# Performance work log

Measured on AMD Instinct MI355X. Metric: run time of the kernel, lower is better.

The kernel has to match this reference:

```python
import jax, jax.numpy as jnp
import numpy as np

N = 100000   # nodes
E = 1600000  # edges (avg degree 16)
F = 128      # num_node_features
H = 128      # hid_size
G = 512      # num graphs in batch
C = 10       # num_classes
D = 32       # graph_degree_distribution.shape[1]
BN_EPS = 1e-5


def setup_inputs() -> dict:
    key = jax.random.key(0)
    ks = jax.random.split(key, 16)
    p = lambda k, shp: jax.random.normal(k, shp, jnp.float32) * 0.02
    x = jax.random.normal(ks[0], (N, F), jnp.float32)
    edge_index = jax.random.randint(ks[1], (2, E), 0, N)
    batch = jnp.sort(jax.random.randint(ks[2], (N,), 0, G))
    degree = jax.random.uniform(ks[3], (N,), jnp.float32) * 10.0
    return dict(
        x=x, edge_index=edge_index, batch=batch, degree=degree,
        eps1=jnp.zeros(()), W1a=p(ks[4], (F, H)), b1a=jnp.zeros(H), W1b=p(ks[5], (H, H)), b1b=jnp.zeros(H),
        g1=jnp.ones(H), be1=jnp.zeros(H),
        eps2=jnp.zeros(()), W2a=p(ks[6], (H, H)), b2a=jnp.zeros(H), W2b=p(ks[7], (H, H)), b2b=jnp.zeros(H),
        g2=jnp.ones(H), be2=jnp.zeros(H),
        Wlin1=p(ks[8], (H, H)), blin1=jnp.zeros(H),
        Wlin2=p(ks[9], (H, C)), blin2=jnp.zeros(C),
        Wlin4=p(ks[10], (H, D)), blin4=jnp.zeros(D),
        Wloss=p(ks[11], (H, 1)), bloss=jnp.zeros(1),
    )


def gin_conv(x, src, dst, eps, Wa, ba, Wb, bb, gamma, beta):
    # GINConv: MLP((1+eps)*x_i + sum_{j->i} x_j); MLP = Lin-ReLU-Lin-ReLU-BN
    agg = jax.ops.segment_sum(x[src], dst, num_segments=x.shape[0])  # [N,F] gather-scatter
    h = (1.0 + eps) * x + agg
    h = jax.nn.relu(h @ Wa + ba)
    h = jax.nn.relu(h @ Wb + bb)
    mu = h.mean(0)
    var = h.var(0)  # biased var, training-mode BN
    return gamma * (h - mu) * jax.lax.rsqrt(var + BN_EPS) + beta


def reference(x, edge_index, batch, degree,
              eps1, W1a, b1a, W1b, b1b, g1, be1,
              eps2, W2a, b2a, W2b, b2b, g2, be2,
              Wlin1, blin1, Wlin2, blin2, Wlin4, blin4, Wloss, bloss):
    src, dst = edge_index[0], edge_index[1]
    h = gin_conv(x, src, dst, eps1, W1a, b1a, W1b, b1b, g1, be1)
    h = gin_conv(h, src, dst, eps2, W2a, b2a, W2b, b2b, g2, be2)
    mse_x = h @ Wloss + bloss                       # [N,1]
    mse_loss = jnp.mean((mse_x - degree[:, None]) ** 2)
    # global_mean_pool over graphs
    sums = jax.ops.segment_sum(h, batch, num_segments=G)
    cnts = jax.ops.segment_sum(jnp.ones((h.shape[0], 1), h.dtype), batch, num_segments=G)
    g = sums / jnp.maximum(cnts, 1.0)               # [G,H]
    z = jax.nn.relu(g @ Wlin1 + blin1)              # dropout inert (eval)
    result1 = jax.nn.log_softmax(z @ Wlin2 + blin2, axis=-1)  # [G,C]
    result3 = z @ Wlin4 + blin4                      # [G,D]
    return result1, result3, mse_loss
```

## Files before the change

### kernel.cpp

```cpp
#include <hip/hip_runtime.h>
#include <hip/hip_bf16.h>

#define HF 128
#define BSH 8
#define BSZ 256
#define NBMAX 1024
#define FCAP 8192
#define HB 512

typedef __attribute__((ext_vector_type(8))) short bf16x8;
typedef __attribute__((ext_vector_type(4))) float f32x4;
typedef __attribute__((ext_vector_type(2))) float f32x2;

__device__ inline float bflo(unsigned u) { return __uint_as_float(u << 16); }
__device__ inline float bfhi(unsigned u) { return __uint_as_float(u & 0xffff0000u); }
__device__ inline unsigned short f2bf(float f) {
    unsigned u = __float_as_uint(f);
    unsigned r = (u + 0x7fffu + ((u >> 16) & 1u)) >> 16;
    return (unsigned short)r;
}
__device__ inline unsigned pack2(float a, float b) {
    return (unsigned)f2bf(a) | ((unsigned)f2bf(b) << 16);
}
__device__ inline uint2 pk8_fp8(const float* v) {
    int a = __builtin_amdgcn_cvt_pk_fp8_f32(v[0], v[1], 0, 0);
    a = __builtin_amdgcn_cvt_pk_fp8_f32(v[2], v[3], a, 1);
    int b = __builtin_amdgcn_cvt_pk_fp8_f32(v[4], v[5], 0, 0);
    b = __builtin_amdgcn_cvt_pk_fp8_f32(v[6], v[7], b, 1);
    uint2 r; r.x = (unsigned)a; r.y = (unsigned)b;
    return r;
}

__global__ __launch_bounds__(256) void init_all(
    const float* __restrict__ x, unsigned short* __restrict__ xb,
    unsigned char* __restrict__ x8, int castBlk, int nchunks,
    const float* __restrict__ w0, const float* __restrict__ w1,
    const float* __restrict__ w2, const float* __restrict__ w3,
    unsigned short* __restrict__ WtAll,
    const int* __restrict__ dst, int* __restrict__ tot, int E, int chunkH,
    const int* __restrict__ batch, int* __restrict__ gstart, int N, int Gn, int nBlocks,
    float* __restrict__ Szero, float* __restrict__ outm)
{
    __shared__ int lh[NBMAX];
    int b = blockIdx.x;
    int t = threadIdx.x;
    if (b < castBlk) {
        int i = b * 256 + t;
        if (i < nchunks) {
            float4 a = ((const float4*)x)[2 * i];
            float4 c = ((const float4*)x)[2 * i + 1];
            uint4 o;
            o.x = pack2(a.x, a.y); o.y = pack2(a.z, a.w);
            o.z = pack2(c.x, c.y); o.w = pack2(c.z, c.w);
            ((uint4*)xb)[i] = o;
            float v[8] = {a.x, a.y, a.z, a.w, c.x, c.y, c.z, c.w};
            ((uint2*)x8)[i] = pk8_fp8(v);
        }
        return;
    }
    b -= castBlk;
    if (b < 4) {
        const float* W = (b == 0) ? w0 : (b == 1) ? w1 : (b == 2) ? w2 : w3;
        unsigned short* O = WtAll + b * 16384;
        for (int idx = t; idx < 16384; idx += 256) {
            int j    = idx & 7;
            int lane = (idx >> 3) & 63;
            int fk   = idx >> 9;
            int kk = fk & 3, nt = fk >> 2;
            int m = lane & 15, quad = lane >> 4;
            int ncol = nt * 16 + m;
            int krow = kk * 32 + quad * 8 + j;
            O[idx] = f2bf(W[krow * 128 + ncol]);
        }
        return;
    }
    b -= 4;
    if (b < HB) {
        int NBl = (N + BSZ - 1) >> BSH;
        for (int i = t; i < NBl; i += 256) lh[i] = 0;
        __syncthreads();
        int beg = b * chunkH;
        int end = min(E, beg + chunkH);
        for (int e = beg + t; e < end; e += 256)
            atomicAdd(&lh[dst[e] >> BSH], 1);
        __syncthreads();
        for (int i = t; i < NBl; i += 256) {
            int c = lh[i];
            if (c) atomicAdd(&tot[i], c);
        }
        return;
    }
    b -= HB;
    if (b < nBlocks) {
        int i = b * 256 + t;
        if (i >= N) return;
        int bi = batch[i];
        int bp = (i == 0) ? -1 : batch[i - 1];
        for (int g = bp + 1; g <= bi; g++) gstart[g] = i;
        if (i == N - 1)
            for (int g = bi + 1; g <= Gn; g++) gstart[g] = N;
        return;
    }
    if (t < 2 * HF) { Szero[t] = 0.f; Szero[t + 2 * HF] = 0.f; }
    if (t == 0) outm[0] = 0.f;
}

__global__ void scanp(const int* __restrict__ tot, int* __restrict__ boff,
                      int* __restrict__ bcur, int NB, int E)
{
    __shared__ int part[256];
    int t = threadIdx.x;
    int v[4];
    int s = 0;
#pragma unroll
    for (int i = 0; i < 4; i++) {
        int idx = t * 4 + i;
        v[i] = (idx < NB) ? tot[idx] : 0;
        s += v[i];
    }
    part[t] = s;
    __syncthreads();
    for (int o = 1; o < 256; o <<= 1) {
        int y = (t >= o) ? part[t - o] : 0;
        __syncthreads();
        part[t] += y;
        __syncthreads();
    }
    int base = part[t] - s;
#pragma unroll
    for (int i = 0; i < 4; i++) {
        int idx = t * 4 + i;
        if (idx < NB) { boff[idx] = base; bcur[idx] = base; base += v[i]; }
    }
    if (t == 0) boff[NB] = E;
}

__global__ __launch_bounds__(256) void bucket_bin(
    const int* __restrict__ src, const int* __restrict__ dst,
    int* __restrict__ bcur, unsigned* __restrict__ ebuf, int E, int NB, int chunkH)
{
    __shared__ int lh[NBMAX];
    int t = threadIdx.x;
    for (int i = t; i < NB; i += 256) lh[i] = 0;
    __syncthreads();
    int beg = blockIdx.x * chunkH;
    int end = min(E, beg + chunkH);
    for (int e = beg + t; e < end; e += 256)
        atomicAdd(&lh[dst[e] >> BSH], 1);
    __syncthreads();
    for (int i = t; i < NB; i += 256) {
        int c = lh[i];
        lh[i] = c ? atomicAdd(&bcur[i], c) : 0;
    }
    __syncthreads();
    for (int e = beg + t; e < end; e += 256) {
        int d = dst[e];
        int b = d >> BSH;
        int pos = atomicAdd(&lh[b], 1);
        ebuf[pos] = ((unsigned)src[e] << BSH) | (unsigned)(d & (BSZ - 1));
    }
}

__global__ __launch_bounds__(256) void bucket_fill(
    const unsigned* __restrict__ ebuf, const int* __restrict__ boff,
    int* __restrict__ off, int* __restrict__ esrc, int N, int NB, int E)
{
    __shared__ int deg[BSZ];
    __shared__ int pref[BSZ];
    __shared__ int lcur[BSZ];
    __shared__ int lsr[FCAP];
    int b = blockIdx.x;
    int t = threadIdx.x;
    int segBeg = boff[b], segEnd = boff[b + 1];
    int segLen = segEnd - segBeg;
    int node0 = b << BSH;
    deg[t] = 0;
    __syncthreads();
    for (int i = segBeg + t; i < segEnd; i += 256)
        atomicAdd(&deg[ebuf[i] & (BSZ - 1)], 1);
    __syncthreads();
    int dv = deg[t];
    pref[t] = dv;
    __syncthreads();
    for (int o = 1; o < 256; o <<= 1) {
        int y = (t >= o) ? pref[t - o] : 0;
        __syncthreads();
        pref[t] += y;
        __syncthreads();
    }
    int excl = pref[t] - dv;
    int node = node0 + t;
    if (node < N) off[node] = segBeg + excl;
    lcur[t] = excl;
    if (b == NB - 1 && t == 0) off[N] = E;
    __syncthreads();
    if (segLen <= FCAP) {
        for (int i = segBeg + t; i < segEnd; i += 256) {
            unsigned v = ebuf[i];
            int slot = atomicAdd(&lcur[v & (BSZ - 1)], 1);
            lsr[slot] = (int)(v >> BSH);
        }
        __syncthreads();
        for (int i = t; i < segLen; i += 256) esrc[segBeg + i] = lsr[i];
    } else {
        for (int i = segBeg + t; i < segEnd; i += 256) {
            unsigned v = ebuf[i];
            int slot = atomicAdd(&lcur[v & (BSZ - 1)], 1);
            esrc[segBeg + slot] = (int)(v >> BSH);
        }
    }
}

template <bool FOLD>
__global__ __launch_bounds__(256, 4) void gather_u(
    const unsigned short* __restrict__ xb, const unsigned char* __restrict__ x8,
    const int* __restrict__ off, const int* __restrict__ esrc,
    const float* __restrict__ epsp,
    const float* __restrict__ S1, const float* __restrict__ S2,
    const float* __restrict__ gamma, const float* __restrict__ beta, float invN,
    unsigned short* __restrict__ Uo, int N)
{
    __shared__ float lsc[HF], lsh[HF];
    int tid = threadIdx.x;
    if (FOLD) {
        if (tid < HF) {
            float mu = S1[tid] * invN;
            float var = S2[tid] * invN - mu * mu;
            float rs = rsqrtf(var + 1e-5f);
            float sc = gamma[tid] * rs;
            lsc[tid] = sc;
            lsh[tid] = beta[tid] - mu * sc;
        }
        __syncthreads();
    }
    int lane16 = tid & 15;
    int node = (blockIdx.x * 256 + tid) >> 4;
    if (node >= N) return;
    int beg = off[node], end = off[node + 1];
    float acc[8] = {0.f, 0.f, 0.f, 0.f, 0.f, 0.f, 0.f, 0.f};
    const unsigned char* x8l = x8 + lane16 * 8;
    for (int j0 = beg; j0 < end; j0 += 16) {
        int myidx = (j0 + lane16 < end) ? esrc[j0 + lane16] : -1;
        uint2 pb[16];
#pragma unroll
        for (int t = 0; t < 16; t++) {
            int s = __shfl(myidx, t, 16);
            int sc = (s < 0) ? 0 : s;
            uint2 pv = *(const uint2*)(x8l + (size_t)sc * HF);
            if (s < 0) { pv.x = 0u; pv.y = 0u; }
            pb[t] = pv;
        }
#pragma unroll
        for (int t = 0; t < 16; t++) {
            f32x2 f0 = __builtin_amdgcn_cvt_pk_f32_fp8((int)pb[t].x, 0);
            f32x2 f1 = __builtin_amdgcn_cvt_pk_f32_fp8((int)pb[t].x, 1);
            f32x2 f2 = __builtin_amdgcn_cvt_pk_f32_fp8((int)pb[t].y, 0);
            f32x2 f3 = __builtin_amdgcn_cvt_pk_f32_fp8((int)pb[t].y, 1);
            acc[0] += f0.x; acc[1] += f0.y;
            acc[2] += f1.x; acc[3] += f1.y;
            acc[4] += f2.x; acc[5] += f2.y;
            acc[6] += f3.x; acc[7] += f3.y;
        }
    }
    float ep = 1.0f + epsp[0];
    uint4 xx = *(const uint4*)(xb + (size_t)node * HF + lane16 * 8);
    acc[0] += ep * bflo(xx.x); acc[1] += ep * bfhi(xx.x);
    acc[2] += ep * bflo(xx.y); acc[3] += ep * bfhi(xx.y);
    acc[4] += ep * bflo(xx.z); acc[5] += ep * bfhi(xx.z);
    acc[6] += ep * bflo(xx.w); acc[7] += ep * bfhi(xx.w);
    if (FOLD) {
        float cf = ep + (float)(end - beg);
        const float4 s0 = *(const float4*)(&lsc[lane16 * 8]);
        const float4 s1 = *(const float4*)(&lsc[lane16 * 8 + 4]);
        const float4 h0 = *(const float4*)(&lsh[lane16 * 8]);
        const float4 h1 = *(const float4*)(&lsh[lane16 * 8 + 4]);
        acc[0] = acc[0] * s0.x + h0.x * cf; acc[1] = acc[1] * s0.y + h0.y * cf;
        acc[2] = acc[2] * s0.z + h0.z * cf; acc[3] = acc[3] * s0.w + h0.w * cf;
        acc[4] = acc[4] * s1.x + h1.x * cf; acc[5] = acc[5] * s1.y + h1.y * cf;
        acc[6] = acc[6] * s1.z + h1.z * cf; acc[7] = acc[7] * s1.w + h1.w * cf;
    }
    uint4 o;
    o.x = pack2(acc[0], acc[1]); o.y = pack2(acc[2], acc[3]);
    o.z = pack2(acc[4], acc[5]); o.w = pack2(acc[6], acc[7]);
    *(uint4*)(Uo + (size_t)node * HF + lane16 * 8) = o;
}

__global__ __launch_bounds__(256, 4) void gemm2L(
    const unsigned short* __restrict__ U,
    const unsigned short* __restrict__ Wfa, const float* __restrict__ ba,
    const unsigned short* __restrict__ Wfb, const float* __restrict__ bb,
    unsigned short* __restrict__ out, unsigned char* __restrict__ out8,
    float* __restrict__ S1, float* __restrict__ S2, int n)
{
    __shared__ __align__(16) unsigned short lT[8192];
    __shared__ float lS1[HF], lS2[HF];
    int tid = threadIdx.x;
    int w = tid >> 6, lane = tid & 63;
    int m = lane & 15, quad = lane >> 4;
    int tile = (blockIdx.x << 2) | w;
    int ntiles = (n + 15) >> 4;
    bool active = tile < ntiles;

    if (tid < HF) { lS1[tid] = 0.f; lS2[tid] = 0.f; }
    __syncthreads();

    if (active) {
        unsigned short* lTw = lT + w * 2048;
        int swzA = (m & 7) << 3;
        int row0 = tile << 4;

        int ar = row0 + m; if (ar >= n) ar = n - 1;
        const unsigned short* up = U + (size_t)ar * HF + quad * 8;
        bf16x8 aF[4];
#pragma unroll
        for (int kk = 0; kk < 4; kk++) aF[kk] = *(const bf16x8*)(up + kk * 32);

        float bav[8], bbv[8];
#pragma unroll
        for (int nt = 0; nt < 8; nt++) { bav[nt] = ba[nt * 16 + m]; bbv[nt] = bb[nt * 16 + m]; }

        const bf16x8* __restrict__ Ba = (const bf16x8*)Wfa;
        const bf16x8* __restrict__ Bb = (const bf16x8*)Wfb;

        f32x4 acc[8];
#pragma unroll
        for (int nt = 0; nt < 8; nt++) acc[nt] = (f32x4){0.f, 0.f, 0.f, 0.f};
#pragma unroll
        for (int nt = 0; nt < 8; nt++) {
#pragma unroll
            for (int kk = 0; kk < 4; kk++) {
                bf16x8 b = Ba[(((nt << 2) | kk) << 6) | lane];
                acc[nt] = __builtin_amdgcn_mfma_f32_16x16x32_bf16(aF[kk], b, acc[nt], 0, 0, 0);
            }
        }
#pragma unroll
        for (int nt = 0; nt < 8; nt++) {
#pragma unroll
            for (int r = 0; r < 4; r++) {
                int row = (quad << 2) | r;
                lTw[(row << 7) | ((nt * 16 + m) ^ ((row & 7) << 3))] =
                    f2bf(fmaxf(acc[nt][r] + bav[nt], 0.f));
            }
        }
        bf16x8 a2[4];
#pragma unroll
        for (int kk = 0; kk < 4; kk++)
            a2[kk] = *(const bf16x8*)(&lTw[(m << 7) | (((kk << 5) | (quad << 3)) ^ swzA)]);
#pragma unroll
        for (int nt = 0; nt < 8; nt++) acc[nt] = (f32x4){0.f, 0.f, 0.f, 0.f};
#pragma unroll
        for (int nt = 0; nt < 8; nt++) {
#pragma unroll
            for (int kk = 0; kk < 4; kk++) {
                bf16x8 b = Bb[(((nt << 2) | kk) << 6) | lane];
                acc[nt] = __builtin_amdgcn_mfma_f32_16x16x32_bf16(a2[kk], b, acc[nt], 0, 0, 0);
            }
        }
#pragma unroll
        for (int nt = 0; nt < 8; nt++) {
            float cs = 0.f, cq = 0.f;
#pragma unroll
            for (int r = 0; r < 4; r++) {
                int row = (quad << 2) | r;
                float v = fmaxf(acc[nt][r] + bbv[nt], 0.f);
                lTw[(row << 7) | ((nt * 16 + m) ^ ((row & 7) << 3))] = f2bf(v);
                if (row0 + row < n) { cs += v; cq += v * v; }
            }
            cs += __shfl_down(cs, 32); cs += __shfl_down(cs, 16);
            cq += __shfl_down(cq, 32); cq += __shfl_down(cq, 16);
            if (quad == 0) {
                atomicAdd(&lS1[nt * 16 + m], cs);
                atomicAdd(&lS2[nt * 16 + m], cq);
            }
        }
#pragma unroll
        for (int i = 0; i < 4; i++) {
            int chunk = (i << 6) | lane;
            int row = chunk >> 4, c16 = chunk & 15;
            int grow = row0 + row;
            if (grow < n) {
                uint4 v = *(const uint4*)(&lTw[(row << 7) | (((c16 << 3) ^ ((row & 7) << 3)))]);
                *(uint4*)(out + (size_t)grow * HF + (c16 << 3)) = v;
                if (out8) {
                    float f[8] = {bflo(v.x), bfhi(v.x), bflo(v.y), bfhi(v.y),
                                  bflo(v.z), bfhi(v.z), bflo(v.w), bfhi(v.w)};
                    *(uint2*)(out8 + (size_t)grow * HF + (c16 << 3)) = pk8_fp8(f);
                }
            }
        }
    }
    __syncthreads();
    if (tid < HF) {
        atomicAdd(&S1[tid], lS1[tid]);
        atomicAdd(&S2[tid], lS2[tid]);
    }
}

__global__ __launch_bounds__(512) void pool_tail(
    const unsigned short* __restrict__ h2raw,
    const float* __restrict__ S1, const float* __restrict__ S2,
    const float* __restrict__ gamma, const float* __restrict__ beta, float invN,
    const int* __restrict__ gstart, const float* __restrict__ W,
    const float* __restrict__ bias,
    const float* __restrict__ Wloss, const float* __restrict__ blossp,
    const float* __restrict__ degree,
    const float* __restrict__ W2, const float* __restrict__ b2,
    const float* __restrict__ W4, const float* __restrict__ b4,
    float* __restrict__ out1, float* __restrict__ out3,
    float* __restrict__ outm, int C_, int D_)
{
    __shared__ float lsc[HF], lsh[HF];
    __shared__ float red[8][HF];
    __shared__ float gv[HF];
    __shared__ float part[4][HF];
    __shared__ float wred[8];
    __shared__ float zz[HF];
    __shared__ float logits[16];
    __shared__ float lse_s;
    int gid = blockIdx.x;
    int t = threadIdx.x;
    if (t < HF) {
        float mu = S1[t] * invN;
        float var = S2[t] * invN - mu * mu;
        float rs = rsqrtf(var + 1e-5f);
        float sc = gamma[t] * rs;
        lsc[t] = sc;
        lsh[t] = beta[t] - mu * sc;
    }
    __syncthreads();
    int c2 = t & 63;
    int rg = t >> 6;
    int b = gstart[gid], e = gstart[gid + 1];
    float wla = lsc[2 * c2] * Wloss[2 * c2];
    float wlb = lsc[2 * c2 + 1] * Wloss[2 * c2 + 1];
    float c0l = lsh[2 * c2] * Wloss[2 * c2] + lsh[2 * c2 + 1] * Wloss[2 * c2 + 1];
    float bl = blossp[0];
    float s0 = 0.f, s1 = 0.f, macc = 0.f;
    for (int r = b + rg; r < e; r += 8) {
        unsigned u = *(const unsigned*)(h2raw + (size_t)r * HF + c2 * 2);
        float v0 = bflo(u), v1 = bfhi(u);
        s0 += v0; s1 += v1;
        float m = v0 * wla + v1 * wlb + c0l;
#pragma unroll
        for (int o = 32; o > 0; o >>= 1) m += __shfl_down(m, o);
        if (c2 == 0) {
            float d = m + bl - degree[r];
            macc += d * d;
        }
    }
    red[rg][c2 * 2] = s0;
    red[rg][c2 * 2 + 1] = s1;
    if (c2 == 0) wred[rg] = macc;
    __syncthreads();
    if (t < HF) {
        float s = red[0][t] + red[1][t] + red[2][t] + red[3][t]
                + red[4][t] + red[5][t] + red[6][t] + red[7][t];
        gv[t] = (e > b) ? lsc[t] * (s / (float)(e - b)) + lsh[t] : 0.f;
    }
    __syncthreads();
    int c = t & 127, kg = t >> 7;
    float a = 0.f;
#pragma unroll 8
    for (int k = kg * 32; k < kg * 32 + 32; k++) a += gv[k] * W[(size_t)k * HF + c];
    part[kg][c] = a;
    __syncthreads();
    if (t < HF) {
        float aa = part[0][t] + part[1][t] + part[2][t] + part[3][t] + bias[t];
        zz[t] = fmaxf(aa, 0.f);
    }
    if (t == 0) {
        float ps = wred[0] + wred[1] + wred[2] + wred[3]
                 + wred[4] + wred[5] + wred[6] + wred[7];
        atomicAdd(outm, ps * invN);
    }
    __syncthreads();
    if (t < C_) {
        float aa = b2[t];
        for (int k = 0; k < HF; k++) aa += zz[k] * W2[(size_t)k * C_ + t];
        logits[t] = aa;
    }
    __syncthreads();
    if (t == 0) {
        float mx = -1e30f;
        for (int i = 0; i < C_; i++) mx = fmaxf(mx, logits[i]);
        float s = 0.f;
        for (int i = 0; i < C_; i++) s += expf(logits[i] - mx);
        lse_s = mx + logf(s);
    }
    __syncthreads();
    if (t < C_) out1[(size_t)gid * C_ + t] = logits[t] - lse_s;
    if (t < D_) {
        float aa = b4[t];
        for (int k = 0; k < HF; k++) aa += zz[k] * W4[(size_t)k * D_ + t];
        out3[(size_t)gid * D_ + t] = aa;
    }
}

extern "C" void kernel_launch(void* const* d_in, const int* in_sizes, int n_in,
                              void* d_out, int out_size, void* d_ws, size_t ws_size,
                              hipStream_t stream)
{
    const float* x      = (const float*)d_in[0];
    const int*   ei     = (const int*)d_in[1];
    const int*   batch  = (const int*)d_in[2];
    const float* degree = (const float*)d_in[3];
    const float* eps1   = (const float*)d_in[4];
    const float* W1a    = (const float*)d_in[5];
    const float* b1a    = (const float*)d_in[6];
    const float* W1b    = (const float*)d_in[7];
    const float* b1b    = (const float*)d_in[8];
    const float* g1     = (const float*)d_in[9];
    const float* be1    = (const float*)d_in[10];
    const float* eps2   = (const float*)d_in[11];
    const float* W2a    = (const float*)d_in[12];
    const float* b2a    = (const float*)d_in[13];
    const float* W2b    = (const float*)d_in[14];
    const float* b2b    = (const float*)d_in[15];
    const float* g2     = (const float*)d_in[16];
    const float* be2    = (const float*)d_in[17];
    const float* Wlin1  = (const float*)d_in[18];
    const float* blin1  = (const float*)d_in[19];
    const float* Wlin2  = (const float*)d_in[20];
    const float* blin2  = (const float*)d_in[21];
    const float* Wlin4  = (const float*)d_in[22];
    const float* blin4  = (const float*)d_in[23];
    const float* Wloss  = (const float*)d_in[24];
    const float* bloss  = (const float*)d_in[25];

    const int N  = in_sizes[0] / HF;
    const int E  = in_sizes[1] / 2;
    const int C_ = in_sizes[21];
    const int D_ = in_sizes[23];
    const int Gn = (out_size - 1) / (C_ + D_);
    const int NB = (N + BSZ - 1) >> BSH;

    const int* src = ei;
    const int* dst = ei + E;

    size_t NH = (size_t)N * HF;
    char* p = (char*)d_ws;
    unsigned short* xb  = (unsigned short*)p; p += NH * 2;
    unsigned short* U   = (unsigned short*)p; p += NH * 2;
    unsigned short* Hp1 = (unsigned short*)p; p += NH * 2;
    unsigned short* Hp2 = (unsigned short*)p; p += NH * 2;
    unsigned char*  x8  = (unsigned char*)p; p += NH;
    unsigned char*  h8  = (unsigned char*)p; p += NH;
    unsigned short* WtAll = (unsigned short*)p; p += 4 * 16384 * 2;
    float* S1a  = (float*)p; p += HF * 4;
    float* S2a  = (float*)p; p += HF * 4;
    float* S1b  = (float*)p; p += HF * 4;
    float* S2b  = (float*)p; p += HF * 4;
    int* gstart = (int*)p; p += (Gn + 1) * 4;
    int* boff   = (int*)p; p += (NBMAX + 1) * 4;
    int* bcur   = (int*)p; p += NBMAX * 4;
    int* tot    = (int*)p; p += NBMAX * 4;
    int* off    = (int*)p; p += (N + 1) * 4;
    int* esrc   = (int*)p; p += E * 4;
    unsigned* ebuf = (unsigned*)p; p += E * 4;

    unsigned short* Wt1a = WtAll;
    unsigned short* Wt1b = WtAll + 16384;
    unsigned short* Wt2a = WtAll + 32768;
    unsigned short* Wt2b = WtAll + 49152;

    float* out1 = (float*)d_out;
    float* out3 = out1 + (size_t)Gn * C_;
    float* outm = out3 + (size_t)Gn * D_;

    int nchunks  = (int)(NH / 8);
    int castBlk  = (nchunks + 255) / 256;
    int nBlocks  = (N + 255) / 256;
    int gatherBlk = (N * 16 + 255) / 256;
    int ntiles   = (N + 15) / 16;
    int gemmBlk  = (ntiles + 3) / 4;
    int chunkH   = (E + HB - 1) / HB;
    float invN = 1.0f / (float)N;

    int initBlk = castBlk + 4 + HB + nBlocks + 1;

    hipMemsetAsync(tot, 0, (size_t)NB * sizeof(int), stream);
    init_all<<<initBlk, 256, 0, stream>>>(x, xb, x8, castBlk, nchunks,
                                          W1a, W1b, W2a, W2b, WtAll,
                                          dst, tot, E, chunkH,
                                          batch, gstart, N, Gn, nBlocks,
                                          S1a, outm);
    scanp<<<1, 256, 0, stream>>>(tot, boff, bcur, NB, E);
    bucket_bin<<<HB, 256, 0, stream>>>(src, dst, bcur, ebuf, E, NB, chunkH);
    bucket_fill<<<NB, 256, 0, stream>>>(ebuf, boff, off, esrc, N, NB, E);
    gather_u<false><<<gatherBlk, 256, 0, stream>>>(xb, x8, off, esrc, eps1,
                                                   nullptr, nullptr, nullptr, nullptr, 0.f, U, N);
    gemm2L<<<gemmBlk, 256, 0, stream>>>(U, Wt1a, b1a, Wt1b, b1b, Hp1, h8, S1a, S2a, N);
    gather_u<true><<<gatherBlk, 256, 0, stream>>>(Hp1, h8, off, esrc, eps2,
                                                  S1a, S2a, g1, be1, invN, U, N);
    gemm2L<<<gemmBlk, 256, 0, stream>>>(U, Wt2a, b2a, Wt2b, b2b, Hp2, nullptr, S1b, S2b, N);
    pool_tail<<<Gn, 512, 0, stream>>>(Hp2, S1b, S2b, g2, be2, invN, gstart,
                                      Wlin1, blin1, Wloss, bloss, degree,
                                      Wlin2, blin2, Wlin4, blin4,
                                      out1, out3, outm, C_, D_);
}
```

Measured before the change: 477.8 us.

## Make gemm2L persistent with weights held in registers split across waves

The fused two-layer GEMM becomes a persistent grid-stride kernel. Each of the 4 waves owns 32 output columns of a shared 16-row tile and keeps its slices of both weight matrices in registers for the whole run, instead of each wave reloading the full weights per tile. BN statistics are accumulated in registers and flushed with one set of global atomics per block. The cost is two __syncthreads per tile, fewer rows in flight per block, and a lower occupancy bound.

```diff
diff --git a/kernel.cpp b/kernel.cpp
--- a/kernel.cpp
+++ b/kernel.cpp
@@ -285,101 +285,100 @@
     *(uint4*)(Uo + (size_t)node * HF + lane16 * 8) = o;
 }
 
-__global__ __launch_bounds__(256, 4) void gemm2L(
+__global__ __launch_bounds__(256, 3) void gemm2L(
     const unsigned short* __restrict__ U,
     const unsigned short* __restrict__ Wfa, const float* __restrict__ ba,
     const unsigned short* __restrict__ Wfb, const float* __restrict__ bb,
     unsigned short* __restrict__ out, unsigned char* __restrict__ out8,
     float* __restrict__ S1, float* __restrict__ S2, int n)
 {
-    __shared__ __align__(16) unsigned short lT[8192];
-    __shared__ float lS1[HF], lS2[HF];
+    __shared__ __align__(16) unsigned short lA[2048];
+    __shared__ __align__(16) unsigned short lB[2048];
     int tid = threadIdx.x;
     int w = tid >> 6, lane = tid & 63;
     int m = lane & 15, quad = lane >> 4;
-    int tile = (blockIdx.x << 2) | w;
+    int swzA = (m & 7) << 3;
     int ntiles = (n + 15) >> 4;
-    bool active = tile < ntiles;
-
-    if (tid < HF) { lS1[tid] = 0.f; lS2[tid] = 0.f; }
-    __syncthreads();
-
-    if (active) {
-        unsigned short* lTw = lT + w * 2048;
-        int swzA = (m & 7) << 3;
+
+    const bf16x8* __restrict__ Ba = (const bf16x8*)Wfa;
+    const bf16x8* __restrict__ Bb = (const bf16x8*)Wfb;
+    bf16x8 wa[2][4], wb[2][4];
+#pragma unroll
+    for (int q = 0; q < 2; q++) {
+        int nt = 2 * w + q;
+#pragma unroll
+        for (int kk = 0; kk < 4; kk++) {
+            wa[q][kk] = Ba[(((nt << 2) | kk) << 6) | lane];
+            wb[q][kk] = Bb[(((nt << 2) | kk) << 6) | lane];
+        }
+    }
+    float bav[2], bbv[2];
+#pragma unroll
+    for (int q = 0; q < 2; q++) {
+        bav[q] = ba[(2 * w + q) * 16 + m];
+        bbv[q] = bb[(2 * w + q) * 16 + m];
+    }
+    float csA[2] = {0.f, 0.f}, cqA[2] = {0.f, 0.f};
+
+    for (int tile = blockIdx.x; tile < ntiles; tile += gridDim.x) {
         int row0 = tile << 4;
-
         int ar = row0 + m; if (ar >= n) ar = n - 1;
         const unsigned short* up = U + (size_t)ar * HF + quad * 8;
         bf16x8 aF[4];
 #pragma unroll
         for (int kk = 0; kk < 4; kk++) aF[kk] = *(const bf16x8*)(up + kk * 32);
 
-        float bav[8], bbv[8];
-#pragma unroll
-        for (int nt = 0; nt < 8; nt++) { bav[nt] = ba[nt * 16 + m]; bbv[nt] = bb[nt * 16 + m]; }
-
-        const bf16x8* __restrict__ Ba = (const bf16x8*)Wfa;
-        const bf16x8* __restrict__ Bb = (const bf16x8*)Wfb;
-
-        f32x4 acc[8];
-#pragma unroll
-        for (int nt = 0; nt < 8; nt++) acc[nt] = (f32x4){0.f, 0.f, 0.f, 0.f};
-#pragma unroll
-        for (int nt = 0; nt < 8; nt++) {
-#pragma unroll
-            for (int kk = 0; kk < 4; kk++) {
-                bf16x8 b = Ba[(((nt << 2) | kk) << 6) | lane];
-                acc[nt] = __builtin_amdgcn_mfma_f32_16x16x32_bf16(aF[kk], b, acc[nt], 0, 0, 0);
-            }
-        }
-#pragma unroll
-        for (int nt = 0; nt < 8; nt++) {
+        f32x4 acc[2];
+#pragma unroll
+        for (int q = 0; q < 2; q++) acc[q] = (f32x4){0.f, 0.f, 0.f, 0.f};
+#pragma unroll
+        for (int q = 0; q < 2; q++)
+#pragma unroll
+            for (int kk = 0; kk < 4; kk++)
+                acc[q] = __builtin_amdgcn_mfma_f32_16x16x32_bf16(aF[kk], wa[q][kk], acc[q], 0, 0, 0);
+#pragma unroll
+        for (int q = 0; q < 2; q++) {
+            int col = (2 * w + q) * 16 + m;
 #pragma unroll
             for (int r = 0; r < 4; r++) {
                 int row = (quad << 2) | r;
-                lTw[(row << 7) | ((nt * 16 + m) ^ ((row & 7) << 3))] =
-                    f2bf(fmaxf(acc[nt][r] + bav[nt], 0.f));
+                lA[(row << 7) | (col ^ ((row & 7) << 3))] =
+                    f2bf(fmaxf(acc[q][r] + bav[q], 0.f));
             }
         }
+        __syncthreads();
         bf16x8 a2[4];
 #pragma unroll
         for (int kk = 0; kk < 4; kk++)
-            a2[kk] = *(const bf16x8*)(&lTw[(m << 7) | (((kk << 5) | (quad << 3)) ^ swzA)]);
-#pragma unroll
-        for (int nt = 0; nt < 8; nt++) acc[nt] = (f32x4){0.f, 0.f, 0.f, 0.f};
-#pragma unroll
-        for (int nt = 0; nt < 8; nt++) {
-#pragma unroll
-            for (int kk = 0; kk < 4; kk++) {
-                bf16x8 b = Bb[(((nt << 2) | kk) << 6) | lane];
-                acc[nt] = __builtin_amdgcn_mfma_f32_16x16x32_bf16(a2[kk], b, acc[nt], 0, 0, 0);
-            }
-        }
-#pragma unroll
-        for (int nt = 0; nt < 8; nt++) {
+            a2[kk] = *(const bf16x8*)(&lA[(m << 7) | (((kk << 5) | (quad << 3)) ^ swzA)]);
+#pragma unroll
+        for (int q = 0; q < 2; q++) acc[q] = (f32x4){0.f, 0.f, 0.f, 0.f};
+#pragma unroll
+        for (int q = 0; q < 2; q++)
+#pragma unroll
+            for (int kk = 0; kk < 4; kk++)
+                acc[q] = __builtin_amdgcn_mfma_f32_16x16x32_bf16(a2[kk], wb[q][kk], acc[q], 0, 0, 0);
+#pragma unroll
+        for (int q = 0; q < 2; q++) {
+            int col = (2 * w + q) * 16 + m;
             float cs = 0.f, cq = 0.f;
 #pragma unroll
             for (int r = 0; r < 4; r++) {
                 int row = (quad << 2) | r;
-                float v = fmaxf(acc[nt][r] + bbv[nt], 0.f);
-                lTw[(row << 7) | ((nt * 16 + m) ^ ((row & 7) << 3))] = f2bf(v);
+                float v = fmaxf(acc[q][r] + bbv[q], 0.f);
+                lB[(row << 7) | (col ^ ((row & 7) << 3))] = f2bf(v);
                 if (row0 + row < n) { cs += v; cq += v * v; }
             }
             cs += __shfl_down(cs, 32); cs += __shfl_down(cs, 16);
             cq += __shfl_down(cq, 32); cq += __shfl_down(cq, 16);
-            if (quad == 0) {
-                atomicAdd(&lS1[nt * 16 + m], cs);
-                atomicAdd(&lS2[nt * 16 + m], cq);
-            }
-        }
-#pragma unroll
-        for (int i = 0; i < 4; i++) {
-            int chunk = (i << 6) | lane;
-            int row = chunk >> 4, c16 = chunk & 15;
+            csA[q] += cs; cqA[q] += cq;
+        }
+        __syncthreads();
+        {
+            int row = tid >> 4, c16 = tid & 15;
             int grow = row0 + row;
             if (grow < n) {
-                uint4 v = *(const uint4*)(&lTw[(row << 7) | (((c16 << 3) ^ ((row & 7) << 3)))]);
+                uint4 v = *(const uint4*)(&lB[(row << 7) | ((c16 << 3) ^ ((row & 7) << 3))]);
                 *(uint4*)(out + (size_t)grow * HF + (c16 << 3)) = v;
                 if (out8) {
                     float f[8] = {bflo(v.x), bfhi(v.x), bflo(v.y), bfhi(v.y),
@@ -389,10 +388,13 @@
             }
         }
     }
-    __syncthreads();
-    if (tid < HF) {
-        atomicAdd(&S1[tid], lS1[tid]);
-        atomicAdd(&S2[tid], lS2[tid]);
+
+    if (quad == 0) {
+#pragma unroll
+        for (int q = 0; q < 2; q++) {
+            atomicAdd(&S1[(2 * w + q) * 16 + m], csA[q]);
+            atomicAdd(&S2[(2 * w + q) * 16 + m], cqA[q]);
+        }
     }
 }
 
@@ -572,7 +574,8 @@
     int nBlocks  = (N + 255) / 256;
     int gatherBlk = (N * 16 + 255) / 256;
     int ntiles   = (N + 15) / 16;
-    int gemmBlk  = (ntiles + 3) / 4;
+    int gemmBlk  = 1024;
+    if (gemmBlk > ntiles) gemmBlk = ntiles;
     int chunkH   = (E + HB - 1) / HB;
     float invN = 1.0f / (float)N;
 
```

Result: faster. 447.2 us (-6.4%).
